# Performance work log

Measured on AMD Instinct MI355X. Metric: run time of the kernel, lower is better.

The kernel has to match this reference:

```python
import jax, jax.numpy as jnp
import numpy as np

B = 16384
TEXT_DIM = 768
AUDIO_DIM = 1024
E = 1024
H = 8
DH = E // H


def setup_inputs() -> dict:
    key = jax.random.key(0)
    ks = jax.random.split(key, 20)
    s_in = lambda d: 1.0 / np.sqrt(d)
    inp = {
        'text_emb': jax.random.normal(ks[0], (B, TEXT_DIM), jnp.float32),
        'audio_emb': jax.random.normal(ks[1], (B, AUDIO_DIM), jnp.float32),
        # modality projections
        'Wt': jax.random.uniform(ks[2], (E, TEXT_DIM), jnp.float32, -s_in(TEXT_DIM), s_in(TEXT_DIM)),
        'bt': jnp.zeros((E,), jnp.float32),
        'Wa': jax.random.uniform(ks[3], (E, AUDIO_DIM), jnp.float32, -s_in(AUDIO_DIM), s_in(AUDIO_DIM)),
        'ba': jnp.zeros((E,), jnp.float32),
        # shared MultiheadAttention (packed in_proj split into q/k/v)
        'Wq': jax.random.uniform(ks[4], (E, E), jnp.float32, -s_in(E), s_in(E)),
        'bq': jnp.zeros((E,), jnp.float32),
        'Wk': jax.random.uniform(ks[5], (E, E), jnp.float32, -s_in(E), s_in(E)),
        'bk': jnp.zeros((E,), jnp.float32),
        'Wv': jax.random.uniform(ks[6], (E, E), jnp.float32, -s_in(E), s_in(E)),
        'bv': jnp.zeros((E,), jnp.float32),
        'Wo': jax.random.uniform(ks[7], (E, E), jnp.float32, -s_in(E), s_in(E)),
        'bo': jnp.zeros((E,), jnp.float32),
        # sigmoid gates
        'Wgt': jax.random.uniform(ks[8], (E, 2 * E), jnp.float32, -s_in(2 * E), s_in(2 * E)),
        'bgt': jnp.zeros((E,), jnp.float32),
        'Wga': jax.random.uniform(ks[9], (E, 2 * E), jnp.float32, -s_in(2 * E), s_in(2 * E)),
        'bga': jnp.zeros((E,), jnp.float32),
    }
    return inp


def _mha(q_in, kv_in, Wq, bq, Wk, bk, Wv, bv, Wo, bo):
    # seq_len == 1 for both query and key/value: tensors are (B, E)
    q = (q_in @ Wq.T + bq).reshape(B, H, DH)
    k = (kv_in @ Wk.T + bk).reshape(B, H, DH)
    v = (kv_in @ Wv.T + bv).reshape(B, H, DH)
    scores = jnp.einsum('bhd,bhd->bh', q, k) / np.sqrt(DH)  # (B, H), single kv slot
    w = jax.nn.softmax(scores[..., None], axis=-1)          # softmax over kv axis (size 1) -> ones
    ctx = (w * v).reshape(B, E)
    return ctx @ Wo.T + bo


def reference(text_emb, audio_emb, Wt, bt, Wa, ba, Wq, bq, Wk, bk, Wv, bv, Wo, bo, Wgt, bgt, Wga, bga):
    t = text_emb @ Wt.T + bt      # (B, E)
    a = audio_emb @ Wa.T + ba     # (B, E)
    t_ctx = _mha(t, a, Wq, bq, Wk, bk, Wv, bv, Wo, bo)
    a_ctx = _mha(a, t, Wq, bq, Wk, bk, Wv, bv, Wo, bo)
    g_t = jax.nn.sigmoid(jnp.concatenate([t, t_ctx], axis=-1) @ Wgt.T + bgt)
    refined_t = g_t * t + (1.0 - g_t) * t_ctx
    g_a = jax.nn.sigmoid(jnp.concatenate([a, a_ctx], axis=-1) @ Wga.T + bga)
    refined_a = g_a * a + (1.0 - g_a) * a_ctx
    return refined_t, refined_a
```

## Files before the change

kernel.cpp:

```cpp
#include <hip/hip_runtime.h>
#include <hip/hip_bf16.h>


typedef __attribute__((ext_vector_type(8))) short short8;
typedef __attribute__((ext_vector_type(4))) float floatx4;

#define WAITV(N) asm volatile("s_waitcnt vmcnt(" #N ")" ::: "memory")
__device__ __forceinline__ void blockbar() {
  asm volatile("" ::: "memory");
  __builtin_amdgcn_s_barrier();
  asm volatile("" ::: "memory");
}

__device__ __forceinline__ float bf2f(__hip_bfloat16 x) { return __bfloat162float(x); }

__device__ __forceinline__ void gl_lds16(const void* g, void* l) {
  __builtin_amdgcn_global_load_lds(
      (const __attribute__((address_space(1))) unsigned int*)g,
      (__attribute__((address_space(3))) unsigned int*)l,
      16, 0, 0);
}

__device__ __forceinline__ void swizzle_mn(int& m_idx, int& n_idx) {
  const int lid = blockIdx.y * 8 + blockIdx.x;
  m_idx = (lid >> 6) * 8 + (lid & 7);
  n_idx = (lid >> 3) & 7;
}

struct CvtJob { const float* src; __hip_bfloat16* dst; int sld, dld, cols4, rowbase; };
struct CvtJobs { CvtJob j[9]; };

__global__ __launch_bounds__(256)
void cvt9_kernel(CvtJobs a) {
  const int r = blockIdx.x;
  int ji = 0;
#pragma unroll
  for (int i = 1; i < 9; ++i) ji += (r >= a.j[i].rowbase) ? 1 : 0;
  const CvtJob J = a.j[ji];
  const int rr = r - J.rowbase;
  const int c4 = threadIdx.x;
  if (c4 >= J.cols4) return;
  const float4 v = *(const float4*)(J.src + (size_t)rr * J.sld + c4 * 4);
  union { __hip_bfloat16 h[4]; uint2 u; } o;
  o.h[0] = __float2bfloat16(v.x);
  o.h[1] = __float2bfloat16(v.y);
  o.h[2] = __float2bfloat16(v.z);
  o.h[3] = __float2bfloat16(v.w);
  *(uint2*)(J.dst + (size_t)rr * J.dld + c4 * 4) = o.u;
}

__global__ __launch_bounds__(256)
void cvt_t_kernel(const float* __restrict__ src, __hip_bfloat16* __restrict__ dst,
                  int R, int C) {
  __shared__ float tile[32][33];
  const int tx = threadIdx.x, ty = threadIdx.y;
  const int bx = blockIdx.x * 32, by = blockIdx.y * 32;
#pragma unroll
  for (int i = 0; i < 32; i += 8)
    tile[ty + i][tx] = src[(size_t)(by + ty + i) * C + bx + tx];
  __syncthreads();
#pragma unroll
  for (int i = 0; i < 32; i += 8)
    dst[(size_t)(bx + ty + i) * R + by + tx] = __float2bfloat16(tile[tx][ty + i]);
}

__global__ __launch_bounds__(256)
void tr_bf16_kernel(const __hip_bfloat16* __restrict__ src,
                    __hip_bfloat16* __restrict__ dst) {
  __shared__ __hip_bfloat16 tile[32][33];
  const int tx = threadIdx.x, ty = threadIdx.y;
  const int bx = blockIdx.x * 32, by = blockIdx.y * 32;
#pragma unroll
  for (int i = 0; i < 32; i += 8)
    tile[ty + i][tx] = src[(size_t)(by + ty + i) * 1024 + bx + tx];
  __syncthreads();
#pragma unroll
  for (int i = 0; i < 32; i += 8)
    dst[(size_t)(bx + ty + i) * 1024 + by + tx] = tile[tx][ty + i];
}

__global__ __launch_bounds__(256)
void mv_kernel(const float* __restrict__ W, int ld, int coff,
               const float* __restrict__ x, const float* __restrict__ b,
               float* __restrict__ y) {
  const int lane = threadIdx.x & 63;
  const int row = blockIdx.x * 4 + (threadIdx.x >> 6);
  float acc = 0.f;
  for (int k = lane; k < 1024; k += 64)
    acc += W[(size_t)row * ld + coff + k] * x[k];
#pragma unroll
  for (int off = 32; off > 0; off >>= 1) acc += __shfl_down(acc, off);
  if (lane == 0) y[row] = acc + b[row];
}

__global__ __launch_bounds__(256)
void mv2_kernel(const float* __restrict__ W0, const float* __restrict__ W1,
                const float* __restrict__ x,
                const float* __restrict__ b0, const float* __restrict__ b1,
                float* __restrict__ y0, float* __restrict__ y1) {
  const float* W = blockIdx.y ? W1 : W0;
  const float* b = blockIdx.y ? b1 : b0;
  float* y = blockIdx.y ? y1 : y0;
  const int lane = threadIdx.x & 63;
  const int row = blockIdx.x * 4 + (threadIdx.x >> 6);
  float acc = 0.f;
  for (int k = lane; k < 1024; k += 64)
    acc += W[(size_t)row * 2048 + 1024 + k] * x[k];
#pragma unroll
  for (int off = 32; off > 0; off >>= 1) acc += __shfl_down(acc, off);
  if (lane == 0) y[row] = acc + b[row];
}

struct GemmJob {
  const __hip_bfloat16* A; const __hip_bfloat16* W;
  const float* bias; __hip_bfloat16* C; int K; int ldc; int coff;
};

__global__ __launch_bounds__(256)
void gemm_bt2_kernel(GemmJob j0, GemmJob j1, int mSplit) {
  constexpr int BK = 32;
  __shared__ __align__(16) __hip_bfloat16 lA[3 * 128 * BK];
  __shared__ __align__(16) __hip_bfloat16 lB[3 * 128 * BK];

  const int tid  = threadIdx.x;
  const int lane = tid & 63;
  const int wave = tid >> 6;
  const int wm = wave & 1;
  const int wn = wave >> 1;
  int m_idx, n_idx;
  swizzle_mn(m_idx, n_idx);
  const bool sec = m_idx >= mSplit;
  const GemmJob J = sec ? j1 : j0;
  const int m0 = (sec ? m_idx - mSplit : m_idx) * 128;
  const int n0 = n_idx * 128;
  const int K = J.K;

  floatx4 acc[4][4];
#pragma unroll
  for (int i = 0; i < 4; ++i)
#pragma unroll
    for (int j = 0; j < 4; ++j) {
      floatx4 z = {0.f, 0.f, 0.f, 0.f};
      acc[i][j] = z;
    }

  const int srow  = tid >> 2;
  const int sc_sw = ((tid & 3) ^ (srow & 3)) * 8;
  const int fr = lane & 15;
  const int fq = (((lane >> 4) ^ (fr & 3))) * 8;

  const __hip_bfloat16* pA = J.A + (size_t)(m0 + srow) * K + sc_sw;
  const __hip_bfloat16* pW = J.W + (size_t)(n0 + srow) * K + sc_sw;
  const size_t SR = (size_t)64 * K;

  int sOff = 0;
  auto stageAB = [&]() {
    gl_lds16(pA,      (char*)lA + sOff + tid * 16);
    gl_lds16(pA + SR, (char*)lA + sOff + 4096 + tid * 16);
    gl_lds16(pW,      (char*)lB + sOff + tid * 16);
    gl_lds16(pW + SR, (char*)lB + sOff + 4096 + tid * 16);
    pA += BK; pW += BK;
    sOff = (sOff == 16384) ? 0 : sOff + 8192;
  };

  auto compute = [&](int cOff) {
    const short* sA = (const short*)((const char*)lA + cOff);
    const short* sB = (const short*)((const char*)lB + cOff);
    short8 af[4], bfr[4];
#pragma unroll
    for (int i = 0; i < 4; ++i)
      af[i] = *(const short8*)(sA + (wm * 64 + i * 16 + fr) * BK + fq);
#pragma unroll
    for (int j = 0; j < 4; ++j)
      bfr[j] = *(const short8*)(sB + (wn * 64 + j * 16 + fr) * BK + fq);
#pragma unroll
    for (int i = 0; i < 4; ++i)
#pragma unroll
      for (int j = 0; j < 4; ++j)
        acc[i][j] = __builtin_amdgcn_mfma_f32_16x16x32_bf16(af[i], bfr[j], acc[i][j], 0, 0, 0);
  };

  const int NT = K / BK;
  int cOff = 0;
  stageAB();
  for (int t = 0; t < NT - 1; ++t) {
    stageAB();
    WAITV(4);
    blockbar();
    compute(cOff);
    cOff = (cOff == 16384) ? 0 : cOff + 8192;
  }
  WAITV(0);
  blockbar();
  compute(cOff);

  const int col = lane & 15;
  const int rq  = (lane >> 4) * 4;
#pragma unroll
  for (int j = 0; j < 4; ++j) {
    const int n = n0 + wn * 64 + j * 16 + col;
    const float bv = J.bias ? J.bias[n] : 0.f;
#pragma unroll
    for (int i = 0; i < 4; ++i)
#pragma unroll
      for (int r = 0; r < 4; ++r) {
        const int m = m0 + wm * 64 + i * 16 + rq + r;
        J.C[(size_t)m * J.ldc + J.coff + n] = __float2bfloat16(acc[i][j][r] + bv);
      }
  }
}

__global__ __launch_bounds__(256)
void fused_gate_kernel(const __hip_bfloat16* __restrict__ Xt,
                       const __hip_bfloat16* __restrict__ Xa,
                       const __hip_bfloat16* __restrict__ Wg1t,
                       const __hip_bfloat16* __restrict__ Wg1a,
                       const __hip_bfloat16* __restrict__ G2vo,
                       const __hip_bfloat16* __restrict__ Wvo,
                       const float* __restrict__ bgt,
                       const float* __restrict__ bga,
                       const float* __restrict__ bvo,
                       float* __restrict__ out) {
  constexpr int BK = 32;
  __shared__ __align__(16) __hip_bfloat16 lA[2 * 128 * BK];
  __shared__ __align__(16) __hip_bfloat16 lB[2 * 128 * BK];
  __shared__ __align__(16) __hip_bfloat16 lC[2 * 128 * BK];

  const int tid  = threadIdx.x;
  const int lane = tid & 63;
  const int wave = tid >> 6;
  const int wm = wave & 1;
  const int wn = wave >> 1;
  int m_idx, n_idx;
  swizzle_mn(m_idx, n_idx);
  const bool aud = m_idx >= 128;
  const int m0 = (m_idx & 127) * 128;
  const int n0 = n_idx * 128;

  const size_t M1 = 1024ull * 1024;
  const __hip_bfloat16* Xs  = aud ? Xa : Xt;
  const __hip_bfloat16* Xo  = aud ? Xt : Xa;
  const __hip_bfloat16* Wg1 = aud ? Wg1a : Wg1t;
  const __hip_bfloat16* Wg2vo = G2vo + (aud ? M1 : 0);
  const float* bg = aud ? bga : bgt;
  float* po = out + (aud ? (size_t)16384 * 1024 : 0);

  floatx4 accL[4][4], accC[4][4];
#pragma unroll
  for (int i = 0; i < 4; ++i)
#pragma unroll
    for (int j = 0; j < 4; ++j) {
      floatx4 z = {0.f, 0.f, 0.f, 0.f};
      accL[i][j] = z;
      accC[i][j] = z;
    }

  const int srow  = tid >> 2;
  const int sc_sw = ((tid & 3) ^ (srow & 3)) * 8;
  const int fr = lane & 15;
  const int fq = (((lane >> 4) ^ (fr & 3))) * 8;

  const __hip_bfloat16* pAs = Xs    + (size_t)(m0 + srow) * 1024 + sc_sw;
  const __hip_bfloat16* pB1 = Wg1   + (size_t)(n0 + srow) * 1024 + sc_sw;
  const __hip_bfloat16* pAo = Xo    + (size_t)(m0 + srow) * 1024 + sc_sw;
  const __hip_bfloat16* pB2 = Wg2vo + (size_t)(n0 + srow) * 1024 + sc_sw;
  const __hip_bfloat16* pBv = Wvo   + (size_t)(n0 + srow) * 1024 + sc_sw;
  const size_t SR = (size_t)64 * 1024;

  auto stage1 = [&](int buf) {
    gl_lds16(pAs,      (char*)lA + buf * 8192 + tid * 16);
    gl_lds16(pAs + SR, (char*)lA + buf * 8192 + 4096 + tid * 16);
    gl_lds16(pB1,      (char*)lB + buf * 8192 + tid * 16);
    gl_lds16(pB1 + SR, (char*)lB + buf * 8192 + 4096 + tid * 16);
    pAs += BK; pB1 += BK;
  };
  auto stage2 = [&](int buf) {
    gl_lds16(pAo,      (char*)lA + buf * 8192 + tid * 16);
    gl_lds16(pAo + SR, (char*)lA + buf * 8192 + 4096 + tid * 16);
    gl_lds16(pB2,      (char*)lB + buf * 8192 + tid * 16);
    gl_lds16(pB2 + SR, (char*)lB + buf * 8192 + 4096 + tid * 16);
    gl_lds16(pBv,      (char*)lC + buf * 8192 + tid * 16);
    gl_lds16(pBv + SR, (char*)lC + buf * 8192 + 4096 + tid * 16);
    pAo += BK; pB2 += BK; pBv += BK;
  };

  auto comp1 = [&](int cur) {
    const short* sA = (const short*)lA + cur * 4096;
    const short* sB = (const short*)lB + cur * 4096;
    short8 af[4], bfr[4];
#pragma unroll
    for (int i = 0; i < 4; ++i)
      af[i] = *(const short8*)(sA + (wm * 64 + i * 16 + fr) * BK + fq);
#pragma unroll
    for (int j = 0; j < 4; ++j)
      bfr[j] = *(const short8*)(sB + (wn * 64 + j * 16 + fr) * BK + fq);
#pragma unroll
    for (int i = 0; i < 4; ++i)
#pragma unroll
      for (int j = 0; j < 4; ++j)
        accL[i][j] = __builtin_amdgcn_mfma_f32_16x16x32_bf16(af[i], bfr[j], accL[i][j], 0, 0, 0);
  };
  auto comp2 = [&](int cur) {
    const short* sA = (const short*)lA + cur * 4096;
    const short* sB = (const short*)lB + cur * 4096;
    const short* sC = (const short*)lC + cur * 4096;
    short8 af[4], bfr[4], cfr[4];
#pragma unroll
    for (int i = 0; i < 4; ++i)
      af[i] = *(const short8*)(sA + (wm * 64 + i * 16 + fr) * BK + fq);
#pragma unroll
    for (int j = 0; j < 4; ++j) {
      bfr[j] = *(const short8*)(sB + (wn * 64 + j * 16 + fr) * BK + fq);
      cfr[j] = *(const short8*)(sC + (wn * 64 + j * 16 + fr) * BK + fq);
    }
#pragma unroll
    for (int i = 0; i < 4; ++i)
#pragma unroll
      for (int j = 0; j < 4; ++j) {
        accL[i][j] = __builtin_amdgcn_mfma_f32_16x16x32_bf16(af[i], bfr[j], accL[i][j], 0, 0, 0);
        accC[i][j] = __builtin_amdgcn_mfma_f32_16x16x32_bf16(af[i], cfr[j], accC[i][j], 0, 0, 0);
      }
  };

  stage1(0);
  for (int t = 0; t < 31; ++t) {
    stage1((t & 1) ^ 1);
    WAITV(4);
    blockbar();
    comp1(t & 1);
    blockbar();
  }
  stage2(0);
  WAITV(6);
  blockbar();
  comp1(1);
  blockbar();
  for (int t = 0; t < 31; ++t) {
    stage2((t & 1) ^ 1);
    WAITV(6);
    blockbar();
    comp2(t & 1);
    blockbar();
  }
  WAITV(0);
  blockbar();
  comp2(1);

  const int col = lane & 15;
  const int rq  = (lane >> 4) * 4;
#pragma unroll
  for (int j = 0; j < 4; ++j) {
    const int n = n0 + wn * 64 + j * 16 + col;
    const float bgv = bg[n];
    const float bcv = bvo[n];
#pragma unroll
    for (int i = 0; i < 4; ++i)
#pragma unroll
      for (int r = 0; r < 4; ++r) {
        const int m = m0 + wm * 64 + i * 16 + rq + r;
        const size_t idx = (size_t)m * 1024 + n;
        const float lg = accL[i][j][r] + bgv;
        const float cv = accC[i][j][r] + bcv;
        const float xv = bf2f(Xs[idx]);
        const float g = 1.f / (1.f + __expf(-lg));
        po[idx] = g * xv + (1.f - g) * cv;
      }
  }
}

extern "C" void kernel_launch(void* const* d_in, const int* in_sizes, int n_in,
                              void* d_out, int out_size, void* d_ws, size_t ws_size,
                              hipStream_t stream) {
  (void)in_sizes; (void)n_in; (void)out_size; (void)ws_size;

  const float* text  = (const float*)d_in[0];
  const float* audio = (const float*)d_in[1];
  const float* Wt  = (const float*)d_in[2];
  const float* bt  = (const float*)d_in[3];
  const float* Wa  = (const float*)d_in[4];
  const float* ba  = (const float*)d_in[5];
  const float* Wv  = (const float*)d_in[10];
  const float* bv  = (const float*)d_in[11];
  const float* Wo  = (const float*)d_in[12];
  const float* bo  = (const float*)d_in[13];
  const float* Wgt = (const float*)d_in[14];
  const float* bgt = (const float*)d_in[15];
  const float* Wga = (const float*)d_in[16];
  const float* bga = (const float*)d_in[17];

  const size_t BE = 16384ull * 1024;
  const size_t M1 = 1024ull * 1024;
  float* out = (float*)d_out;

  __hip_bfloat16* p = (__hip_bfloat16*)d_ws;
  __hip_bfloat16* X      = p; p += 2 * BE;
  __hip_bfloat16* Wt_b   = p; p += 768ull * 1024;
  __hip_bfloat16* Wa_b   = p; p += M1;
  __hip_bfloat16* Wo_b   = p; p += M1;
  __hip_bfloat16* Wvo_b  = p; p += M1;
  __hip_bfloat16* Wg1t_b = p; p += M1;
  __hip_bfloat16* Wg1a_b = p; p += M1;
  __hip_bfloat16* G2vo   = p; p += 2 * M1;
  float* bvo  = (float*)p;
  float* bgtp = bvo + 1024;
  float* bgap = bvo + 2048;

  __hip_bfloat16* scr     = (__hip_bfloat16*)d_out;
  __hip_bfloat16* text_b  = scr;
  __hip_bfloat16* audio_b = scr + 16384ull * 768;
  __hip_bfloat16* WvT_b   = audio_b + BE;
  __hip_bfloat16* WvoT_b  = WvT_b + M1;
  __hip_bfloat16* G2      = WvoT_b + M1;

  dim3 blk(256, 1, 1);

  CvtJobs cj;
  cj.j[0] = { text,       text_b,  768,  768,  192, 0 };
  cj.j[1] = { audio,      audio_b, 1024, 1024, 256, 16384 };
  cj.j[2] = { Wt,         Wt_b,    1024, 1024, 256, 32768 };
  cj.j[3] = { Wa,         Wa_b,    1024, 1024, 256, 33536 };
  cj.j[4] = { Wo,         Wo_b,    1024, 1024, 256, 34560 };
  cj.j[5] = { Wgt,        Wg1t_b,  2048, 1024, 256, 35584 };
  cj.j[6] = { Wgt + 1024, G2,      2048, 1024, 256, 36608 };
  cj.j[7] = { Wga,        Wg1a_b,  2048, 1024, 256, 37632 };
  cj.j[8] = { Wga + 1024, G2 + M1, 2048, 1024, 256, 38656 };
  cvt9_kernel<<<dim3(39680), blk, 0, stream>>>(cj);
  cvt_t_kernel<<<dim3(32, 32), dim3(32, 8), 0, stream>>>(Wv, WvT_b, 1024, 1024);

  mv_kernel<<<dim3(256), blk, 0, stream>>>(Wo, 1024, 0, bv, bo, bvo);
  mv2_kernel<<<dim3(256, 2), blk, 0, stream>>>(Wgt, Wga, bvo, bgt, bga, bgtp, bgap);

  GemmJob f1 = { Wo_b, WvT_b, nullptr, Wvo_b, 1024, 1024, 0 };
  gemm_bt2_kernel<<<dim3(8, 8), blk, 0, stream>>>(f1, f1, 999);
  tr_bf16_kernel<<<dim3(32, 32), dim3(32, 8), 0, stream>>>(Wvo_b, WvoT_b);
  GemmJob f3 = { G2, WvoT_b, nullptr, G2vo, 1024, 1024, 0 };
  gemm_bt2_kernel<<<dim3(8, 16), blk, 0, stream>>>(f3, f3, 999);

  GemmJob pt = { text_b,  Wt_b, bt, X,      768,  1024, 0 };
  GemmJob pa = { audio_b, Wa_b, ba, X + BE, 1024, 1024, 0 };
  gemm_bt2_kernel<<<dim3(8, 256), blk, 0, stream>>>(pt, pa, 128);

  fused_gate_kernel<<<dim3(8, 256), blk, 0, stream>>>(
      X, X + BE, Wg1t_b, Wg1a_b, G2vo, Wvo_b, bgtp, bgap, bvo, out);
}
```

Before: 639.9 us.

## Load weight fragments directly from global into registers, bypassing LDS staging

In both GEMM kernels the weight (B) operand fragments are now read straight from global memory into registers each k-step, and only the activation (A) tile is staged through LDS. The fused gate kernel also moves from a double-buffered LDS ring with two barriers per step to a triple-buffered ring with one barrier. The aim is to cut LDS traffic, LDS footprint and barrier count. In exchange, weight loads are duplicated across waves that share columns and are not tile-coalesced. Their latency also sits on the MFMA critical path, because the compiler must wait on the register loads, which were issued after the A prefetch.

```diff
diff --git a/kernel.cpp b/kernel.cpp
--- a/kernel.cpp
+++ b/kernel.cpp
@@ -120,7 +120,6 @@
 void gemm_bt2_kernel(GemmJob j0, GemmJob j1, int mSplit) {
   constexpr int BK = 32;
   __shared__ __align__(16) __hip_bfloat16 lA[3 * 128 * BK];
-  __shared__ __align__(16) __hip_bfloat16 lB[3 * 128 * BK];
 
   const int tid  = threadIdx.x;
   const int lane = tid & 63;
@@ -146,53 +145,58 @@
 
   const int srow  = tid >> 2;
   const int sc_sw = ((tid & 3) ^ (srow & 3)) * 8;
-  const int fr = lane & 15;
-  const int fq = (((lane >> 4) ^ (fr & 3))) * 8;
+  const int fr  = lane & 15;
+  const int fqs = (((lane >> 4) ^ (fr & 3))) * 8;
+  const int fqg = (lane >> 4) * 8;
 
   const __hip_bfloat16* pA = J.A + (size_t)(m0 + srow) * K + sc_sw;
-  const __hip_bfloat16* pW = J.W + (size_t)(n0 + srow) * K + sc_sw;
+  const __hip_bfloat16* Wb = J.W + (size_t)n0 * K;
+  int ob = (wn * 64 + fr) * K + fqg;
   const size_t SR = (size_t)64 * K;
 
-  int sOff = 0;
-  auto stageAB = [&]() {
+  int sOff = 0, cOff = 0;
+  auto stageA = [&]() {
     gl_lds16(pA,      (char*)lA + sOff + tid * 16);
     gl_lds16(pA + SR, (char*)lA + sOff + 4096 + tid * 16);
-    gl_lds16(pW,      (char*)lB + sOff + tid * 16);
-    gl_lds16(pW + SR, (char*)lB + sOff + 4096 + tid * 16);
-    pA += BK; pW += BK;
+    pA += BK;
     sOff = (sOff == 16384) ? 0 : sOff + 8192;
   };
 
-  auto compute = [&](int cOff) {
+  short8 bfr[4];
+  auto loadB = [&]() {
+#pragma unroll
+    for (int j = 0; j < 4; ++j)
+      bfr[j] = *(const short8*)(Wb + j * 16 * K + ob);
+    ob += 32;
+  };
+
+  auto compute = [&]() {
     const short* sA = (const short*)((const char*)lA + cOff);
-    const short* sB = (const short*)((const char*)lB + cOff);
-    short8 af[4], bfr[4];
-#pragma unroll
-    for (int i = 0; i < 4; ++i)
-      af[i] = *(const short8*)(sA + (wm * 64 + i * 16 + fr) * BK + fq);
-#pragma unroll
-    for (int j = 0; j < 4; ++j)
-      bfr[j] = *(const short8*)(sB + (wn * 64 + j * 16 + fr) * BK + fq);
+    short8 af[4];
+#pragma unroll
+    for (int i = 0; i < 4; ++i)
+      af[i] = *(const short8*)(sA + (wm * 64 + i * 16 + fr) * BK + fqs);
 #pragma unroll
     for (int i = 0; i < 4; ++i)
 #pragma unroll
       for (int j = 0; j < 4; ++j)
         acc[i][j] = __builtin_amdgcn_mfma_f32_16x16x32_bf16(af[i], bfr[j], acc[i][j], 0, 0, 0);
+    cOff = (cOff == 16384) ? 0 : cOff + 8192;
   };
 
   const int NT = K / BK;
-  int cOff = 0;
-  stageAB();
+  stageA();
   for (int t = 0; t < NT - 1; ++t) {
-    stageAB();
-    WAITV(4);
+    stageA();
+    loadB();
+    WAITV(6);
     blockbar();
-    compute(cOff);
-    cOff = (cOff == 16384) ? 0 : cOff + 8192;
+    compute();
   }
-  WAITV(0);
+  loadB();
+  WAITV(4);
   blockbar();
-  compute(cOff);
+  compute();
 
   const int col = lane & 15;
   const int rq  = (lane >> 4) * 4;
@@ -222,9 +226,7 @@
                        const float* __restrict__ bvo,
                        float* __restrict__ out) {
   constexpr int BK = 32;
-  __shared__ __align__(16) __hip_bfloat16 lA[2 * 128 * BK];
-  __shared__ __align__(16) __hip_bfloat16 lB[2 * 128 * BK];
-  __shared__ __align__(16) __hip_bfloat16 lC[2 * 128 * BK];
+  __shared__ __align__(16) __hip_bfloat16 lA[3 * 128 * BK];
 
   const int tid  = threadIdx.x;
   const int lane = tid & 63;
@@ -238,10 +240,11 @@
   const int n0 = n_idx * 128;
 
   const size_t M1 = 1024ull * 1024;
-  const __hip_bfloat16* Xs  = aud ? Xa : Xt;
-  const __hip_bfloat16* Xo  = aud ? Xt : Xa;
-  const __hip_bfloat16* Wg1 = aud ? Wg1a : Wg1t;
-  const __hip_bfloat16* Wg2vo = G2vo + (aud ? M1 : 0);
+  const __hip_bfloat16* Xs   = aud ? Xa : Xt;
+  const __hip_bfloat16* Xo   = aud ? Xt : Xa;
+  const __hip_bfloat16* Wg1B = (aud ? Wg1a : Wg1t) + (size_t)n0 * 1024;
+  const __hip_bfloat16* Wg2B = G2vo + (aud ? M1 : 0) + (size_t)n0 * 1024;
+  const __hip_bfloat16* WvoB = Wvo + (size_t)n0 * 1024;
   const float* bg = aud ? bga : bgt;
   float* po = out + (aud ? (size_t)16384 * 1024 : 0);
 
@@ -257,62 +260,66 @@
 
   const int srow  = tid >> 2;
   const int sc_sw = ((tid & 3) ^ (srow & 3)) * 8;
-  const int fr = lane & 15;
-  const int fq = (((lane >> 4) ^ (fr & 3))) * 8;
-
-  const __hip_bfloat16* pAs = Xs    + (size_t)(m0 + srow) * 1024 + sc_sw;
-  const __hip_bfloat16* pB1 = Wg1   + (size_t)(n0 + srow) * 1024 + sc_sw;
-  const __hip_bfloat16* pAo = Xo    + (size_t)(m0 + srow) * 1024 + sc_sw;
-  const __hip_bfloat16* pB2 = Wg2vo + (size_t)(n0 + srow) * 1024 + sc_sw;
-  const __hip_bfloat16* pBv = Wvo   + (size_t)(n0 + srow) * 1024 + sc_sw;
+  const int fr  = lane & 15;
+  const int fqs = (((lane >> 4) ^ (fr & 3))) * 8;
+  const int fqg = (lane >> 4) * 8;
+
+  const __hip_bfloat16* pAs = Xs + (size_t)(m0 + srow) * 1024 + sc_sw;
+  const __hip_bfloat16* pAo = Xo + (size_t)(m0 + srow) * 1024 + sc_sw;
   const size_t SR = (size_t)64 * 1024;
 
-  auto stage1 = [&](int buf) {
-    gl_lds16(pAs,      (char*)lA + buf * 8192 + tid * 16);
-    gl_lds16(pAs + SR, (char*)lA + buf * 8192 + 4096 + tid * 16);
-    gl_lds16(pB1,      (char*)lB + buf * 8192 + tid * 16);
-    gl_lds16(pB1 + SR, (char*)lB + buf * 8192 + 4096 + tid * 16);
-    pAs += BK; pB1 += BK;
-  };
-  auto stage2 = [&](int buf) {
-    gl_lds16(pAo,      (char*)lA + buf * 8192 + tid * 16);
-    gl_lds16(pAo + SR, (char*)lA + buf * 8192 + 4096 + tid * 16);
-    gl_lds16(pB2,      (char*)lB + buf * 8192 + tid * 16);
-    gl_lds16(pB2 + SR, (char*)lB + buf * 8192 + 4096 + tid * 16);
-    gl_lds16(pBv,      (char*)lC + buf * 8192 + tid * 16);
-    gl_lds16(pBv + SR, (char*)lC + buf * 8192 + 4096 + tid * 16);
-    pAo += BK; pB2 += BK; pBv += BK;
-  };
-
-  auto comp1 = [&](int cur) {
-    const short* sA = (const short*)lA + cur * 4096;
-    const short* sB = (const short*)lB + cur * 4096;
-    short8 af[4], bfr[4];
-#pragma unroll
-    for (int i = 0; i < 4; ++i)
-      af[i] = *(const short8*)(sA + (wm * 64 + i * 16 + fr) * BK + fq);
+  int sOff = 0, cOff = 0;
+  auto stage1 = [&]() {
+    gl_lds16(pAs,      (char*)lA + sOff + tid * 16);
+    gl_lds16(pAs + SR, (char*)lA + sOff + 4096 + tid * 16);
+    pAs += BK;
+    sOff = (sOff == 16384) ? 0 : sOff + 8192;
+  };
+  auto stage2 = [&]() {
+    gl_lds16(pAo,      (char*)lA + sOff + tid * 16);
+    gl_lds16(pAo + SR, (char*)lA + sOff + 4096 + tid * 16);
+    pAo += BK;
+    sOff = (sOff == 16384) ? 0 : sOff + 8192;
+  };
+
+  int ob1 = (wn * 64 + fr) * 1024 + fqg;
+  int ob2 = ob1;
+
+  short8 bfr[4], cfr[4];
+  auto loadB1 = [&]() {
 #pragma unroll
     for (int j = 0; j < 4; ++j)
-      bfr[j] = *(const short8*)(sB + (wn * 64 + j * 16 + fr) * BK + fq);
+      bfr[j] = *(const short8*)(Wg1B + j * 16384 + ob1);
+    ob1 += 32;
+  };
+  auto loadB2 = [&]() {
+#pragma unroll
+    for (int j = 0; j < 4; ++j) {
+      bfr[j] = *(const short8*)(Wg2B + j * 16384 + ob2);
+      cfr[j] = *(const short8*)(WvoB + j * 16384 + ob2);
+    }
+    ob2 += 32;
+  };
+
+  auto comp1 = [&]() {
+    const short* sA = (const short*)((const char*)lA + cOff);
+    short8 af[4];
+#pragma unroll
+    for (int i = 0; i < 4; ++i)
+      af[i] = *(const short8*)(sA + (wm * 64 + i * 16 + fr) * BK + fqs);
 #pragma unroll
     for (int i = 0; i < 4; ++i)
 #pragma unroll
       for (int j = 0; j < 4; ++j)
         accL[i][j] = __builtin_amdgcn_mfma_f32_16x16x32_bf16(af[i], bfr[j], accL[i][j], 0, 0, 0);
-  };
-  auto comp2 = [&](int cur) {
-    const short* sA = (const short*)lA + cur * 4096;
-    const short* sB = (const short*)lB + cur * 4096;
-    const short* sC = (const short*)lC + cur * 4096;
-    short8 af[4], bfr[4], cfr[4];
-#pragma unroll
-    for (int i = 0; i < 4; ++i)
-      af[i] = *(const short8*)(sA + (wm * 64 + i * 16 + fr) * BK + fq);
-#pragma unroll
-    for (int j = 0; j < 4; ++j) {
-      bfr[j] = *(const short8*)(sB + (wn * 64 + j * 16 + fr) * BK + fq);
-      cfr[j] = *(const short8*)(sC + (wn * 64 + j * 16 + fr) * BK + fq);
-    }
+    cOff = (cOff == 16384) ? 0 : cOff + 8192;
+  };
+  auto comp2 = [&]() {
+    const short* sA = (const short*)((const char*)lA + cOff);
+    short8 af[4];
+#pragma unroll
+    for (int i = 0; i < 4; ++i)
+      af[i] = *(const short8*)(sA + (wm * 64 + i * 16 + fr) * BK + fqs);
 #pragma unroll
     for (int i = 0; i < 4; ++i)
 #pragma unroll
@@ -320,31 +327,33 @@
         accL[i][j] = __builtin_amdgcn_mfma_f32_16x16x32_bf16(af[i], bfr[j], accL[i][j], 0, 0, 0);
         accC[i][j] = __builtin_amdgcn_mfma_f32_16x16x32_bf16(af[i], cfr[j], accC[i][j], 0, 0, 0);
       }
-  };
-
-  stage1(0);
+    cOff = (cOff == 16384) ? 0 : cOff + 8192;
+  };
+
+  stage1();
   for (int t = 0; t < 31; ++t) {
-    stage1((t & 1) ^ 1);
-    WAITV(4);
+    stage1();
+    loadB1();
+    WAITV(6);
     blockbar();
-    comp1(t & 1);
-    blockbar();
+    comp1();
   }
-  stage2(0);
+  stage2();
+  loadB1();
   WAITV(6);
   blockbar();
-  comp1(1);
+  comp1();
+  for (int t = 0; t < 31; ++t) {
+    stage2();
+    loadB2();
+    WAITV(10);
+    blockbar();
+    comp2();
+  }
+  loadB2();
+  WAITV(8);
   blockbar();
-  for (int t = 0; t < 31; ++t) {
-    stage2((t & 1) ^ 1);
-    WAITV(6);
-    blockbar();
-    comp2(t & 1);
-    blockbar();
-  }
-  WAITV(0);
-  blockbar();
-  comp2(1);
+  comp2();
 
   const int col = lane & 15;
   const int rq  = (lane >> 4) * 4;
```

Result: slower. 852.2 us (+33.2%).

## Batch projection and weight-fold GEMMs into one launch, triple-buffer gate kernel

Applied to the files above, without the earlier changes.

Merges the text/audio projection GEMMs and the Wo·Wv weight-fold GEMMs into a single four-job launch. The transpose kernel is dropped by computing the transposed product directly as a second GEMM job. The fused gate kernel moves from double-buffered LDS with two barriers per step to a triple-buffered LDS ring with one barrier per step, so loads can overlap compute more. This removes launch and tail overhead at the cost of more LDS per block (72KB), which may lower occupancy.

```diff
diff --git a/kernel.cpp b/kernel.cpp
--- a/kernel.cpp
+++ b/kernel.cpp
@@ -65,21 +65,6 @@
 }
 
 __global__ __launch_bounds__(256)
-void tr_bf16_kernel(const __hip_bfloat16* __restrict__ src,
-                    __hip_bfloat16* __restrict__ dst) {
-  __shared__ __hip_bfloat16 tile[32][33];
-  const int tx = threadIdx.x, ty = threadIdx.y;
-  const int bx = blockIdx.x * 32, by = blockIdx.y * 32;
-#pragma unroll
-  for (int i = 0; i < 32; i += 8)
-    tile[ty + i][tx] = src[(size_t)(by + ty + i) * 1024 + bx + tx];
-  __syncthreads();
-#pragma unroll
-  for (int i = 0; i < 32; i += 8)
-    dst[(size_t)(bx + ty + i) * 1024 + by + tx] = tile[tx][ty + i];
-}
-
-__global__ __launch_bounds__(256)
 void mv_kernel(const float* __restrict__ W, int ld, int coff,
                const float* __restrict__ x, const float* __restrict__ b,
                float* __restrict__ y) {
@@ -117,7 +102,8 @@
 };
 
 __global__ __launch_bounds__(256)
-void gemm_bt2_kernel(GemmJob j0, GemmJob j1, int mSplit) {
+void gemm_bt4_kernel(GemmJob j0, GemmJob j1, GemmJob j2, GemmJob j3,
+                     int c1, int c2, int c3) {
   constexpr int BK = 32;
   __shared__ __align__(16) __hip_bfloat16 lA[3 * 128 * BK];
   __shared__ __align__(16) __hip_bfloat16 lB[3 * 128 * BK];
@@ -129,9 +115,12 @@
   const int wn = wave >> 1;
   int m_idx, n_idx;
   swizzle_mn(m_idx, n_idx);
-  const bool sec = m_idx >= mSplit;
-  const GemmJob J = sec ? j1 : j0;
-  const int m0 = (sec ? m_idx - mSplit : m_idx) * 128;
+  GemmJob J; int mb;
+  if (m_idx < c1)      { J = j0; mb = m_idx; }
+  else if (m_idx < c2) { J = j1; mb = m_idx - c1; }
+  else if (m_idx < c3) { J = j2; mb = m_idx - c2; }
+  else                 { J = j3; mb = m_idx - c3; }
+  const int m0 = mb * 128;
   const int n0 = n_idx * 128;
   const int K = J.K;
 
@@ -147,7 +136,7 @@
   const int srow  = tid >> 2;
   const int sc_sw = ((tid & 3) ^ (srow & 3)) * 8;
   const int fr = lane & 15;
-  const int fq = (((lane >> 4) ^ (fr & 3))) * 8;
+  const int fqs = (((lane >> 4) ^ (fr & 3))) * 8;
 
   const __hip_bfloat16* pA = J.A + (size_t)(m0 + srow) * K + sc_sw;
   const __hip_bfloat16* pW = J.W + (size_t)(n0 + srow) * K + sc_sw;
@@ -163,36 +152,36 @@
     sOff = (sOff == 16384) ? 0 : sOff + 8192;
   };
 
-  auto compute = [&](int cOff) {
+  int cOff = 0;
+  auto compute = [&]() {
     const short* sA = (const short*)((const char*)lA + cOff);
     const short* sB = (const short*)((const char*)lB + cOff);
     short8 af[4], bfr[4];
 #pragma unroll
     for (int i = 0; i < 4; ++i)
-      af[i] = *(const short8*)(sA + (wm * 64 + i * 16 + fr) * BK + fq);
+      af[i] = *(const short8*)(sA + (wm * 64 + i * 16 + fr) * BK + fqs);
 #pragma unroll
     for (int j = 0; j < 4; ++j)
-      bfr[j] = *(const short8*)(sB + (wn * 64 + j * 16 + fr) * BK + fq);
+      bfr[j] = *(const short8*)(sB + (wn * 64 + j * 16 + fr) * BK + fqs);
 #pragma unroll
     for (int i = 0; i < 4; ++i)
 #pragma unroll
       for (int j = 0; j < 4; ++j)
         acc[i][j] = __builtin_amdgcn_mfma_f32_16x16x32_bf16(af[i], bfr[j], acc[i][j], 0, 0, 0);
+    cOff = (cOff == 16384) ? 0 : cOff + 8192;
   };
 
   const int NT = K / BK;
-  int cOff = 0;
   stageAB();
   for (int t = 0; t < NT - 1; ++t) {
     stageAB();
     WAITV(4);
     blockbar();
-    compute(cOff);
-    cOff = (cOff == 16384) ? 0 : cOff + 8192;
+    compute();
   }
   WAITV(0);
   blockbar();
-  compute(cOff);
+  compute();
 
   const int col = lane & 15;
   const int rq  = (lane >> 4) * 4;
@@ -222,9 +211,8 @@
                        const float* __restrict__ bvo,
                        float* __restrict__ out) {
   constexpr int BK = 32;
-  __shared__ __align__(16) __hip_bfloat16 lA[2 * 128 * BK];
-  __shared__ __align__(16) __hip_bfloat16 lB[2 * 128 * BK];
-  __shared__ __align__(16) __hip_bfloat16 lC[2 * 128 * BK];
+  constexpr int BUF = 24576;
+  __shared__ __align__(16) __hip_bfloat16 lds[3 * 12288];
 
   const int tid  = threadIdx.x;
   const int lane = tid & 63;
@@ -258,7 +246,7 @@
   const int srow  = tid >> 2;
   const int sc_sw = ((tid & 3) ^ (srow & 3)) * 8;
   const int fr = lane & 15;
-  const int fq = (((lane >> 4) ^ (fr & 3))) * 8;
+  const int fqs = (((lane >> 4) ^ (fr & 3))) * 8;
 
   const __hip_bfloat16* pAs = Xs    + (size_t)(m0 + srow) * 1024 + sc_sw;
   const __hip_bfloat16* pB1 = Wg1   + (size_t)(n0 + srow) * 1024 + sc_sw;
@@ -267,51 +255,55 @@
   const __hip_bfloat16* pBv = Wvo   + (size_t)(n0 + srow) * 1024 + sc_sw;
   const size_t SR = (size_t)64 * 1024;
 
-  auto stage1 = [&](int buf) {
-    gl_lds16(pAs,      (char*)lA + buf * 8192 + tid * 16);
-    gl_lds16(pAs + SR, (char*)lA + buf * 8192 + 4096 + tid * 16);
-    gl_lds16(pB1,      (char*)lB + buf * 8192 + tid * 16);
-    gl_lds16(pB1 + SR, (char*)lB + buf * 8192 + 4096 + tid * 16);
+  int sOff = 0, cOff = 0;
+  auto stage1 = [&]() {
+    gl_lds16(pAs,      (char*)lds + sOff + tid * 16);
+    gl_lds16(pAs + SR, (char*)lds + sOff + 4096 + tid * 16);
+    gl_lds16(pB1,      (char*)lds + sOff + 8192 + tid * 16);
+    gl_lds16(pB1 + SR, (char*)lds + sOff + 12288 + tid * 16);
     pAs += BK; pB1 += BK;
-  };
-  auto stage2 = [&](int buf) {
-    gl_lds16(pAo,      (char*)lA + buf * 8192 + tid * 16);
-    gl_lds16(pAo + SR, (char*)lA + buf * 8192 + 4096 + tid * 16);
-    gl_lds16(pB2,      (char*)lB + buf * 8192 + tid * 16);
-    gl_lds16(pB2 + SR, (char*)lB + buf * 8192 + 4096 + tid * 16);
-    gl_lds16(pBv,      (char*)lC + buf * 8192 + tid * 16);
-    gl_lds16(pBv + SR, (char*)lC + buf * 8192 + 4096 + tid * 16);
+    sOff = (sOff == 2 * BUF) ? 0 : sOff + BUF;
+  };
+  auto stage2 = [&]() {
+    gl_lds16(pAo,      (char*)lds + sOff + tid * 16);
+    gl_lds16(pAo + SR, (char*)lds + sOff + 4096 + tid * 16);
+    gl_lds16(pB2,      (char*)lds + sOff + 8192 + tid * 16);
+    gl_lds16(pB2 + SR, (char*)lds + sOff + 12288 + tid * 16);
+    gl_lds16(pBv,      (char*)lds + sOff + 16384 + tid * 16);
+    gl_lds16(pBv + SR, (char*)lds + sOff + 20480 + tid * 16);
     pAo += BK; pB2 += BK; pBv += BK;
-  };
-
-  auto comp1 = [&](int cur) {
-    const short* sA = (const short*)lA + cur * 4096;
-    const short* sB = (const short*)lB + cur * 4096;
+    sOff = (sOff == 2 * BUF) ? 0 : sOff + BUF;
+  };
+
+  auto comp1 = [&]() {
+    const short* sA = (const short*)((const char*)lds + cOff);
+    const short* sB = (const short*)((const char*)lds + cOff + 8192);
     short8 af[4], bfr[4];
 #pragma unroll
     for (int i = 0; i < 4; ++i)
-      af[i] = *(const short8*)(sA + (wm * 64 + i * 16 + fr) * BK + fq);
+      af[i] = *(const short8*)(sA + (wm * 64 + i * 16 + fr) * BK + fqs);
 #pragma unroll
     for (int j = 0; j < 4; ++j)
-      bfr[j] = *(const short8*)(sB + (wn * 64 + j * 16 + fr) * BK + fq);
+      bfr[j] = *(const short8*)(sB + (wn * 64 + j * 16 + fr) * BK + fqs);
 #pragma unroll
     for (int i = 0; i < 4; ++i)
 #pragma unroll
       for (int j = 0; j < 4; ++j)
         accL[i][j] = __builtin_amdgcn_mfma_f32_16x16x32_bf16(af[i], bfr[j], accL[i][j], 0, 0, 0);
-  };
-  auto comp2 = [&](int cur) {
-    const short* sA = (const short*)lA + cur * 4096;
-    const short* sB = (const short*)lB + cur * 4096;
-    const short* sC = (const short*)lC + cur * 4096;
+    cOff = (cOff == 2 * BUF) ? 0 : cOff + BUF;
+  };
+  auto comp2 = [&]() {
+    const short* sA = (const short*)((const char*)lds + cOff);
+    const short* sB = (const short*)((const char*)lds + cOff + 8192);
+    const short* sC = (const short*)((const char*)lds + cOff + 16384);
     short8 af[4], bfr[4], cfr[4];
 #pragma unroll
     for (int i = 0; i < 4; ++i)
-      af[i] = *(const short8*)(sA + (wm * 64 + i * 16 + fr) * BK + fq);
+      af[i] = *(const short8*)(sA + (wm * 64 + i * 16 + fr) * BK + fqs);
 #pragma unroll
     for (int j = 0; j < 4; ++j) {
-      bfr[j] = *(const short8*)(sB + (wn * 64 + j * 16 + fr) * BK + fq);
-      cfr[j] = *(const short8*)(sC + (wn * 64 + j * 16 + fr) * BK + fq);
+      bfr[j] = *(const short8*)(sB + (wn * 64 + j * 16 + fr) * BK + fqs);
+      cfr[j] = *(const short8*)(sC + (wn * 64 + j * 16 + fr) * BK + fqs);
     }
 #pragma unroll
     for (int i = 0; i < 4; ++i)
@@ -320,31 +312,29 @@
         accL[i][j] = __builtin_amdgcn_mfma_f32_16x16x32_bf16(af[i], bfr[j], accL[i][j], 0, 0, 0);
         accC[i][j] = __builtin_amdgcn_mfma_f32_16x16x32_bf16(af[i], cfr[j], accC[i][j], 0, 0, 0);
       }
-  };
-
-  stage1(0);
+    cOff = (cOff == 2 * BUF) ? 0 : cOff + BUF;
+  };
+
+  stage1();
   for (int t = 0; t < 31; ++t) {
-    stage1((t & 1) ^ 1);
+    stage1();
     WAITV(4);
     blockbar();
-    comp1(t & 1);
-    blockbar();
+    comp1();
   }
-  stage2(0);
+  stage2();
   WAITV(6);
   blockbar();
-  comp1(1);
-  blockbar();
+  comp1();
   for (int t = 0; t < 31; ++t) {
-    stage2((t & 1) ^ 1);
+    stage2();
     WAITV(6);
     blockbar();
-    comp2(t & 1);
-    blockbar();
+    comp2();
   }
   WAITV(0);
   blockbar();
-  comp2(1);
+  comp2();
 
   const int col = lane & 15;
   const int rq  = (lane >> 4) * 4;
@@ -430,15 +420,14 @@
   mv_kernel<<<dim3(256), blk, 0, stream>>>(Wo, 1024, 0, bv, bo, bvo);
   mv2_kernel<<<dim3(256, 2), blk, 0, stream>>>(Wgt, Wga, bvo, bgt, bga, bgtp, bgap);
 
-  GemmJob f1 = { Wo_b, WvT_b, nullptr, Wvo_b, 1024, 1024, 0 };
-  gemm_bt2_kernel<<<dim3(8, 8), blk, 0, stream>>>(f1, f1, 999);
-  tr_bf16_kernel<<<dim3(32, 32), dim3(32, 8), 0, stream>>>(Wvo_b, WvoT_b);
+  GemmJob pt = { text_b,  Wt_b,  bt,      X,       768,  1024, 0 };
+  GemmJob pa = { audio_b, Wa_b,  ba,      X + BE,  1024, 1024, 0 };
+  GemmJob f1 = { Wo_b,    WvT_b, nullptr, Wvo_b,   1024, 1024, 0 };
+  GemmJob f2 = { WvT_b,   Wo_b,  nullptr, WvoT_b,  1024, 1024, 0 };
+  gemm_bt4_kernel<<<dim3(8, 272), blk, 0, stream>>>(pt, pa, f1, f2, 128, 256, 264);
+
   GemmJob f3 = { G2, WvoT_b, nullptr, G2vo, 1024, 1024, 0 };
-  gemm_bt2_kernel<<<dim3(8, 16), blk, 0, stream>>>(f3, f3, 999);
-
-  GemmJob pt = { text_b,  Wt_b, bt, X,      768,  1024, 0 };
-  GemmJob pa = { audio_b, Wa_b, ba, X + BE, 1024, 1024, 0 };
-  gemm_bt2_kernel<<<dim3(8, 256), blk, 0, stream>>>(pt, pa, 128);
+  gemm_bt4_kernel<<<dim3(8, 16), blk, 0, stream>>>(f3, f3, f3, f3, 999, 999, 999);
 
   fused_gate_kernel<<<dim3(8, 256), blk, 0, stream>>>(
       X, X + BE, Wg1t_b, Wg1a_b, G2vo, Wvo_b, bgtp, bgap, bvo, out);
```

After: 601.5 us. 6.0% less time.
